# Kernel optimization log

Measured on AMD Instinct MI355X. Metric: run time of the kernel, lower is better.

## Reference

```python
import jax, jax.numpy as jnp
import numpy as np

B, C, H, W = 4, 64, 160, 160
K = 3
KK = K * K
PAD = (K - 1) // 2
EPS = 1e-5


def conv2d(x, w, b):
    y = jax.lax.conv_general_dilated(
        x, w, (1, 1), [(PAD, PAD), (PAD, PAD)],
        dimension_numbers=('NCHW', 'OIHW', 'NCHW'))
    return y + b[None, :, None, None]


def batchnorm(x, g, b, m, v):
    # eval-mode BN with running stats
    return (x - m[None, :, None, None]) * jax.lax.rsqrt(v + EPS)[None, :, None, None] * g[None, :, None, None] + b[None, :, None, None]


def bilinear_gather(x, py, px):
    # x: [B,C,H,W]; py,px: [B,KK,H,W] float sample coords -> [B,C,KK,H,W]
    Bx, Cx, Hx, Wx = x.shape
    y0 = jnp.floor(py)
    x0 = jnp.floor(px)
    ly = py - y0
    lx = px - x0
    x_flat = x.reshape(Bx, Cx, 1, Hx * Wx)
    acc = jnp.zeros((Bx, Cx, py.shape[1], Hx * Wx), dtype=x.dtype)
    corners = ((y0, x0, (1 - ly) * (1 - lx)),
               (y0, x0 + 1, (1 - ly) * lx),
               (y0 + 1, x0, ly * (1 - lx)),
               (y0 + 1, x0 + 1, ly * lx))
    for yi, xi, wgt in corners:
        valid = (yi >= 0) & (yi < Hx) & (xi >= 0) & (xi < Wx)
        yc = jnp.clip(yi, 0, Hx - 1).astype(jnp.int32)
        xc = jnp.clip(xi, 0, Wx - 1).astype(jnp.int32)
        idx = (yc * Wx + xc).reshape(Bx, -1, Hx * Wx)          # [B,KK,HW]
        g = jnp.take_along_axis(x_flat, idx[:, None], axis=3)  # [B,C,KK,HW]
        acc = acc + (wgt * valid).reshape(Bx, 1, -1, Hx * Wx) * g
    return acc.reshape(Bx, Cx, -1, Hx, Wx)


def modulated_deform_conv(x, offset, mask, weight):
    # x:[B,C,H,W] offset:[B,2*KK,H,W] (mmcv layout: pairs (dy,dx) interleaved) mask:[B,KK,H,W]
    Bx, Cx, Hx, Wx = x.shape
    Co = weight.shape[0]
    off = offset.reshape(Bx, KK, 2, Hx, Wx)
    k = jnp.arange(KK)
    ki = (k // K).astype(x.dtype)
    kj = (k % K).astype(x.dtype)
    ys = jnp.arange(Hx, dtype=x.dtype)
    xs = jnp.arange(Wx, dtype=x.dtype)
    py = ys[None, None, :, None] - PAD + ki[None, :, None, None] + off[:, :, 0]
    px = xs[None, None, None, :] - PAD + kj[None, :, None, None] + off[:, :, 1]
    samp = bilinear_gather(x, py, px)            # [B,C,KK,H,W]
    samp = samp * mask[:, None]                  # modulation
    return jnp.einsum('bckhw,ock->bohw', samp, weight.reshape(Co, Cx, KK))


def setup_inputs() -> dict:
    key = jax.random.key(0)
    ks = jax.random.split(key, 16)
    inp = {
        'x': jax.random.normal(ks[0], (B, C, H, W), jnp.float32),
        'w_om1': jax.random.normal(ks[1], (3 * KK, C, K, K), jnp.float32) * 0.01,
        'b_om1': jax.random.normal(ks[2], (3 * KK,), jnp.float32) * 0.01,
        'w_dcn1': jax.random.normal(ks[3], (C, C, K, K), jnp.float32) * 0.04,
        'bn1_g': jax.random.uniform(ks[4], (C,), jnp.float32, 0.5, 1.5),
        'bn1_b': jax.random.normal(ks[5], (C,), jnp.float32) * 0.1,
        'bn1_m': jax.random.normal(ks[6], (C,), jnp.float32) * 0.1,
        'bn1_v': jax.random.uniform(ks[7], (C,), jnp.float32, 0.5, 1.5),
        'w_om2': jax.random.normal(ks[8], (3 * KK, C, K, K), jnp.float32) * 0.01,
        'b_om2': jax.random.normal(ks[9], (3 * KK,), jnp.float32) * 0.01,
        'w_dcn2': jax.random.normal(ks[10], (C, C, K, K), jnp.float32) * 0.04,
        'bn2_g': jax.random.uniform(ks[11], (C,), jnp.float32, 0.5, 1.5),
        'bn2_b': jax.random.normal(ks[12], (C,), jnp.float32) * 0.1,
        'bn2_m': jax.random.normal(ks[13], (C,), jnp.float32) * 0.1,
        'bn2_v': jax.random.uniform(ks[14], (C,), jnp.float32, 0.5, 1.5),
    }
    return inp


def reference(x, w_om1, b_om1, w_dcn1, bn1_g, bn1_b, bn1_m, bn1_v,
              w_om2, b_om2, w_dcn2, bn2_g, bn2_b, bn2_m, bn2_v):
    identity = x
    om1 = conv2d(x, w_om1, b_om1)
    o1, o2, m1 = jnp.split(om1, 3, axis=1)
    offset1 = jnp.concatenate([o1, o2], axis=1)
    mask1 = jax.nn.sigmoid(m1)
    out = modulated_deform_conv(x, offset1, mask1, w_dcn1)
    out = batchnorm(out, bn1_g, bn1_b, bn1_m, bn1_v)
    out = jax.nn.gelu(out, approximate=False)
    om2 = conv2d(out, w_om2, b_om2)
    o1b, o2b, m2 = jnp.split(om2, 3, axis=1)
    offset2 = jnp.concatenate([o1b, o2b], axis=1)
    mask2 = jax.nn.sigmoid(m2)
    out = modulated_deform_conv(out, offset2, mask2, w_dcn2)
    out = batchnorm(out, bn2_g, bn2_b, bn2_m, bn2_v)
    out = out + identity
    return jax.nn.gelu(out, approximate=False)
```

## Files before the change

kernel.cpp:

```cpp
#include <hip/hip_runtime.h>
#include <math.h>

#define HH 160
#define WW 160
#define HWSZ 25600
#define TR 14
#define TC 22
#define NSLOT 308

typedef __attribute__((ext_vector_type(8))) short short8;
typedef __attribute__((ext_vector_type(4))) short short4v;
typedef __attribute__((ext_vector_type(8))) _Float16 half8;
typedef __attribute__((ext_vector_type(2))) _Float16 half2v;
typedef __attribute__((ext_vector_type(4))) float f32x4;
typedef __attribute__((ext_vector_type(16))) float f32x16;

__device__ __forceinline__ short f2h(float f) {
  union { _Float16 h; short s; } u; u.h = (_Float16)f; return u.s;
}
__device__ __forceinline__ float h2f(short s) {
  union { _Float16 h; short s; } u; u.s = s; return (float)u.h;
}
__device__ __forceinline__ half2v bcast_h(short s) {
  unsigned int x = (unsigned short)s; x |= x << 16;
  union { unsigned int u; half2v h; } v; v.u = x; return v.h;
}

__global__ __launch_bounds__(256) void pre_kernel(
    const float* __restrict__ x,
    const float* __restrict__ g1, const float* __restrict__ b1,
    const float* __restrict__ m1, const float* __restrict__ v1,
    const float* __restrict__ g2, const float* __restrict__ b2,
    const float* __restrict__ m2, const float* __restrict__ v2,
    const float* __restrict__ wd1, const float* __restrict__ wd2,
    const float* __restrict__ wo1, const float* __restrict__ wo2,
    float* __restrict__ sc, short* __restrict__ wd1h, short* __restrict__ wd2h,
    short* __restrict__ wo1h, short* __restrict__ wo2h,
    short* __restrict__ xcl) {
  __shared__ short tmp[64][72];
  int t = threadIdx.x;
  int bx = blockIdx.x;
  if (bx < 1600) {
    int b = bx / 400, p0 = (bx - b * 400) * 64;
    const float* xb = x + (size_t)b * 64 * HWSZ;
    for (int i = t; i < 4096; i += 256) {
      int c = i >> 6, p = i & 63;
      tmp[p][c] = f2h(xb[c * HWSZ + p0 + p]);
    }
    __syncthreads();
    short* ob = xcl + ((size_t)b * HWSZ + p0) * 64;
    for (int i = t; i < 512; i += 256) {
      int p = i >> 3, g = i & 7;
      *(short8*)&ob[p * 64 + g * 8] = *(const short8*)&tmp[p][g * 8];
    }
    return;
  }
  int i0 = (bx - 1600) * 256 + t;
  for (int i = i0; i < 36864; i += 16384) {
    int j = i & 7, oc = (i >> 3) & 31, hi = (i >> 8) & 1;
    int ot = (i >> 9) & 1, s = (i >> 10) & 3, tap = i >> 12;
    int src = (ot * 32 + oc) * 576 + (s * 16 + hi * 8 + j) * 9 + tap;
    wd1h[i] = f2h(wd1[src]);
    wd2h[i] = f2h(wd2[src]);
  }
  for (int i = i0; i < 18432; i += 16384) {
    int j = i & 7, q = (i >> 3) & 3, m = (i >> 5) & 15;
    int ot = (i >> 9) & 1, f = i >> 10;
    int kp = f * 32 + q * 8 + j;
    int k = kp >> 6, c = kp & 63;
    int oc = ot * 16 + m;
    wo1h[i] = (oc < 27) ? f2h(wo1[oc * 576 + c * 9 + k]) : (short)0;
    wo2h[i] = (oc < 27) ? f2h(wo2[oc * 576 + c * 9 + k]) : (short)0;
  }
  if (i0 < 64) {
    float s1 = g1[i0] * rsqrtf(v1[i0] + 1e-5f);
    sc[i0]       = s1;
    sc[64 + i0]  = b1[i0] - m1[i0] * s1;
    float s2 = g2[i0] * rsqrtf(v2[i0] + 1e-5f);
    sc[128 + i0] = s2;
    sc[192 + i0] = b2[i0] - m2[i0] * s2;
  }
}

__global__ __launch_bounds__(256, 2) void dcn_fused(
    const short* __restrict__ xcl,
    const short* __restrict__ who,
    const float* __restrict__ bias_om,
    const short* __restrict__ whd,
    const float* __restrict__ scale, const float* __restrict__ shift,
    const short* __restrict__ id_cl,
    short* __restrict__ out_cl,
    float* __restrict__ out_f32) {
  __shared__ short xt[NSLOT * 64];
  __shared__ __align__(16) short wA[12288];
  __shared__ __align__(16) short oms[4608];

  int t = threadIdx.x;
  int x0 = blockIdx.x * 16, y0 = blockIdx.y * 8, b = blockIdx.z;
  int w = t >> 6, lane = t & 63, q = lane >> 4, m = lane & 15;
  int hi = lane >> 5, p31 = lane & 31;
  int ybase = y0 - 3, xbase = x0 - 3;

  short8 pr[6];
#pragma unroll
  for (int c = 0; c < 6; c++)
    pr[c] = *(const short8*)&whd[c * 2048 + t * 8];

  const short* xb = xcl + (size_t)b * HWSZ * 64;
  for (int i = t; i < NSLOT * 8; i += 256) {
    int slot = i >> 3, g = i & 7;
    int ty = slot / TC, tx = slot - ty * TC;
    int gy = ybase + ty, gx = xbase + tx;
    short8 v = {};
    if (gy >= 0 && gy < HH && gx >= 0 && gx < WW)
      v = *(const short8*)&xb[(gy * WW + gx) * 64 + g * 8];
    *(short8*)&xt[slot * 64 + ((g ^ (slot & 7)) << 3)] = v;
  }
#pragma unroll
  for (int c = 0; c < 6; c++)
    *(short8*)&wA[c * 2048 + t * 8] = pr[c];
#pragma unroll
  for (int c = 0; c < 6; c++)
    pr[c] = *(const short8*)&whd[12288 + c * 2048 + t * 8];
  __syncthreads();

  {
    f32x4 oacc[2][2] = {};
#pragma unroll 6
    for (int f = 0; f < 18; f++) {
      int k = f >> 1;
      int ki = k / 3, kj = k - ki * 3;
      int g = (f & 1) * 4 + q;
      const short* ap = who + (f * 128 + m * 4 + q) * 8;
      short8 a0 = *(const short8*)ap;
      short8 a1 = *(const short8*)(ap + 512);
      union { short8 s8; half8 h; } A0, A1;
      A0.s8 = a0; A1.s8 = a1;
#pragma unroll
      for (int p = 0; p < 2; p++) {
        int slotb = (w * 2 + p + ki + 2) * TC + (m + kj + 2);
        union { short8 s8; half8 h; } B;
        B.s8 = *(const short8*)&xt[slotb * 64 + ((g ^ (slotb & 7)) << 3)];
        oacc[p][0] = __builtin_amdgcn_mfma_f32_16x16x32_f16(A0.h, B.h, oacc[p][0], 0, 0, 0);
        oacc[p][1] = __builtin_amdgcn_mfma_f32_16x16x32_f16(A1.h, B.h, oacc[p][1], 0, 0, 0);
      }
    }
#pragma unroll
    for (int p = 0; p < 2; p++) {
      int px = w * 32 + p * 16 + m;
#pragma unroll
      for (int mt = 0; mt < 2; mt++) {
        short4v pv;
#pragma unroll
        for (int r = 0; r < 4; r++) {
          int oc = mt * 16 + q * 4 + r;
          float bb = (oc < 27) ? bias_om[oc] : 0.f;
          pv[r] = f2h(oacc[p][mt][r] + bb);
        }
        *(short4v*)&oms[px * 36 + mt * 16 + q * 4] = pv;
      }
    }
  }
  __syncthreads();

  union { short s[36]; short4v v4[9]; } omr;
  {
    int px = w * 32 + p31;
#pragma unroll
    for (int i = 0; i < 9; i++)
      omr.v4[i] = *(const short4v*)&oms[px * 36 + i * 4];
  }

  int y = y0 + w * 2 + (p31 >> 4), x = x0 + m;

  short4v ivs[8];
  if (out_f32) {
    size_t pbase = ((size_t)b * HWSZ + y * WW + x) * 64;
#pragma unroll
    for (int ot = 0; ot < 2; ot++)
#pragma unroll
      for (int blk = 0; blk < 4; blk++)
        ivs[ot * 4 + blk] =
            *(const short4v*)&id_cl[pbase + ot * 32 + blk * 8 + hi * 4];
  }

  f32x16 acc0 = {}, acc1 = {};
#pragma unroll
  for (int grp = 0; grp < 3; ++grp) {
    if (grp > 0) {
      __syncthreads();
#pragma unroll
      for (int c = 0; c < 6; c++)
        *(short8*)&wA[c * 2048 + t * 8] = pr[c];
      if (grp < 2) {
#pragma unroll
        for (int c = 0; c < 6; c++)
          pr[c] = *(const short8*)&whd[(grp + 1) * 12288 + c * 2048 + t * 8];
      }
      __syncthreads();
    }
#pragma unroll
    for (int kt = 0; kt < 3; ++kt) {
      const int k = grp * 3 + kt;
      float dy = h2f(omr.s[2 * k]);
      float dx = h2f(omr.s[2 * k + 1]);
      float ml = h2f(omr.s[18 + k]);
      float msk = 1.f / (1.f + __expf(-ml));
      int ki = k / 3, kj = k - ki * 3;
      float py  = (float)(y - 1 + ki) + dy;
      float pxf = (float)(x - 1 + kj) + dx;
      float fy = floorf(py), fx = floorf(pxf);
      float ly = py - fy, lx = pxf - fx;
      int yi0 = (int)fy, xi0 = (int)fx;
      bool vy0 = (yi0 >= 0) & (yi0 < HH), vy1 = (yi0 + 1 >= 0) & (yi0 + 1 < HH);
      bool vx0 = (xi0 >= 0) & (xi0 < WW), vx1 = (xi0 + 1 >= 0) & (xi0 + 1 < WW);
      int ty0 = min(max(yi0 - ybase, 0), TR - 2);
      int tx0 = min(max(xi0 - xbase, 0), TC - 2);
      int p00 = ty0 * TC + tx0;
      half2v w00 = bcast_h(f2h((vy0 & vx0) ? (1.f - ly) * (1.f - lx) * msk : 0.f));
      half2v w01 = bcast_h(f2h((vy0 & vx1) ? (1.f - ly) * lx * msk : 0.f));
      half2v w10 = bcast_h(f2h((vy1 & vx0) ? ly * (1.f - lx) * msk : 0.f));
      half2v w11 = bcast_h(f2h((vy1 & vx1) ? ly * lx * msk : 0.f));
      int s00 = p00, s01 = p00 + 1, s10 = p00 + TC, s11 = p00 + TC + 1;
#pragma unroll
      for (int s = 0; s < 4; s++) {
        int g = s * 2 + hi;
        union { short8 s8; half2v h[4]; } c00, c01, c10, c11, bb;
        c00.s8 = *(const short8*)&xt[s00 * 64 + ((g ^ (s00 & 7)) << 3)];
        c01.s8 = *(const short8*)&xt[s01 * 64 + ((g ^ (s01 & 7)) << 3)];
        c10.s8 = *(const short8*)&xt[s10 * 64 + ((g ^ (s10 & 7)) << 3)];
        c11.s8 = *(const short8*)&xt[s11 * 64 + ((g ^ (s11 & 7)) << 3)];
#pragma unroll
        for (int d = 0; d < 4; d++)
          bb.h[d] = c00.h[d] * w00 + c01.h[d] * w01 + c10.h[d] * w10 +
                    c11.h[d] * w11;
        const short* ap = wA + kt * 4096 + s * 1024 + lane * 8;
        short8 a0 = *(const short8*)ap;
        short8 a1 = *(const short8*)(ap + 512);
        union { short8 s8; half8 h8; } B, A0, A1;
        B.s8 = bb.s8; A0.s8 = a0; A1.s8 = a1;
        acc0 = __builtin_amdgcn_mfma_f32_32x32x16_f16(A0.h8, B.h8, acc0, 0, 0, 0);
        acc1 = __builtin_amdgcn_mfma_f32_32x32x16_f16(A1.h8, B.h8, acc1, 0, 0, 0);
      }
    }
  }

  if (out_f32) {
#pragma unroll
    for (int ot = 0; ot < 2; ot++) {
#pragma unroll
      for (int r = 0; r < 16; r++) {
        int oc = ot * 32 + (r & 3) + 8 * (r >> 2) + 4 * hi;
        float a = ot ? acc1[r] : acc0[r];
        size_t idx = ((size_t)(b * 64 + oc)) * HWSZ + y * WW + x;
        float v = a * scale[oc] + shift[oc] + h2f(ivs[ot * 4 + (r >> 2)][r & 3]);
        v = 0.5f * v * (1.f + erff(v * 0.70710678118654752f));
        out_f32[idx] = v;
      }
    }
  } else {
    size_t base = ((size_t)b * HWSZ + y * WW + x) * 64;
#pragma unroll
    for (int ot = 0; ot < 2; ot++) {
#pragma unroll
      for (int blk = 0; blk < 4; blk++) {
        short4v pv;
#pragma unroll
        for (int rr = 0; rr < 4; rr++) {
          int r = blk * 4 + rr;
          int oc = ot * 32 + blk * 8 + hi * 4 + rr;
          float a = ot ? acc1[r] : acc0[r];
          float v = a * scale[oc] + shift[oc];
          v = 0.5f * v * (1.f + erff(v * 0.70710678118654752f));
          pv[rr] = f2h(v);
        }
        *(short4v*)&out_cl[base + ot * 32 + blk * 8 + hi * 4] = pv;
      }
    }
  }
}

extern "C" void kernel_launch(void* const* d_in, const int* in_sizes, int n_in,
                              void* d_out, int out_size, void* d_ws, size_t ws_size,
                              hipStream_t stream) {
  const float* x     = (const float*)d_in[0];
  const float* w_om1 = (const float*)d_in[1];
  const float* b_om1 = (const float*)d_in[2];
  const float* w_d1  = (const float*)d_in[3];
  const float* bn1g  = (const float*)d_in[4];
  const float* bn1b  = (const float*)d_in[5];
  const float* bn1m  = (const float*)d_in[6];
  const float* bn1v  = (const float*)d_in[7];
  const float* w_om2 = (const float*)d_in[8];
  const float* b_om2 = (const float*)d_in[9];
  const float* w_d2  = (const float*)d_in[10];
  const float* bn2g  = (const float*)d_in[11];
  const float* bn2b  = (const float*)d_in[12];
  const float* bn2m  = (const float*)d_in[13];
  const float* bn2v  = (const float*)d_in[14];

  float* ws    = (float*)d_ws;
  float* sc    = ws;
  short* w1h   = (short*)(ws + 256);
  short* w2h   = w1h + 36864;
  short* wo1h  = w2h + 36864;
  short* wo2h  = wo1h + 18432;
  short* x_cl  = (short*)(ws + 55552);
  short* o1_cl = x_cl + 6553600;
  float* outp  = (float*)d_out;

  pre_kernel<<<dim3(1664), dim3(256), 0, stream>>>(
      x, bn1g, bn1b, bn1m, bn1v, bn2g, bn2b, bn2m, bn2v,
      w_d1, w_d2, w_om1, w_om2, sc, w1h, w2h, wo1h, wo2h, x_cl);

  dim3 grid(WW / 16, HH / 8, 4);
  dcn_fused<<<grid, dim3(256), 0, stream>>>(
      x_cl, wo1h, b_om1, w1h, sc, sc + 64, nullptr, o1_cl, nullptr);
  dcn_fused<<<grid, dim3(256), 0, stream>>>(
      o1_cl, wo2h, b_om2, w2h, sc + 128, sc + 192, x_cl, nullptr, outp);
}
```

Measured before the change: 209.0 us.

## Shrink weight staging to one tap and union LDS to fit three blocks per CU

```diff
diff --git a/kernel.cpp b/kernel.cpp
--- a/kernel.cpp
+++ b/kernel.cpp
@@ -82,7 +82,7 @@
   }
 }
 
-__global__ __launch_bounds__(256, 2) void dcn_fused(
+__global__ __launch_bounds__(256, 3) void dcn_fused(
     const short* __restrict__ xcl,
     const short* __restrict__ who,
     const float* __restrict__ bias_om,
@@ -92,8 +92,7 @@
     short* __restrict__ out_cl,
     float* __restrict__ out_f32) {
   __shared__ short xt[NSLOT * 64];
-  __shared__ __align__(16) short wA[12288];
-  __shared__ __align__(16) short oms[4608];
+  __shared__ __align__(16) short uni[5120];
 
   int t = threadIdx.x;
   int x0 = blockIdx.x * 16, y0 = blockIdx.y * 8, b = blockIdx.z;
@@ -101,10 +100,8 @@
   int hi = lane >> 5, p31 = lane & 31;
   int ybase = y0 - 3, xbase = x0 - 3;
 
-  short8 pr[6];
-#pragma unroll
-  for (int c = 0; c < 6; c++)
-    pr[c] = *(const short8*)&whd[c * 2048 + t * 8];
+  short8 pr0 = *(const short8*)&whd[t * 8];
+  short8 pr1 = *(const short8*)&whd[2048 + t * 8];
 
   const short* xb = xcl + (size_t)b * HWSZ * 64;
   for (int i = t; i < NSLOT * 8; i += 256) {
@@ -116,12 +113,6 @@
       v = *(const short8*)&xb[(gy * WW + gx) * 64 + g * 8];
     *(short8*)&xt[slot * 64 + ((g ^ (slot & 7)) << 3)] = v;
   }
-#pragma unroll
-  for (int c = 0; c < 6; c++)
-    *(short8*)&wA[c * 2048 + t * 8] = pr[c];
-#pragma unroll
-  for (int c = 0; c < 6; c++)
-    pr[c] = *(const short8*)&whd[12288 + c * 2048 + t * 8];
   __syncthreads();
 
   {
@@ -157,19 +148,26 @@
           float bb = (oc < 27) ? bias_om[oc] : 0.f;
           pv[r] = f2h(oacc[p][mt][r] + bb);
         }
-        *(short4v*)&oms[px * 36 + mt * 16 + q * 4] = pv;
+        *(short4v*)&uni[px * 40 + mt * 16 + q * 4] = pv;
       }
     }
   }
   __syncthreads();
 
-  union { short s[36]; short4v v4[9]; } omr;
+  union { short s[40]; short8 v8[5]; } omr;
   {
     int px = w * 32 + p31;
 #pragma unroll
-    for (int i = 0; i < 9; i++)
-      omr.v4[i] = *(const short4v*)&oms[px * 36 + i * 4];
-  }
+    for (int i = 0; i < 5; i++)
+      omr.v8[i] = *(const short8*)&uni[px * 40 + i * 8];
+  }
+  __syncthreads();
+
+  *(short8*)&uni[t * 8]        = pr0;
+  *(short8*)&uni[2048 + t * 8] = pr1;
+  pr0 = *(const short8*)&whd[4096 + t * 8];
+  pr1 = *(const short8*)&whd[4096 + 2048 + t * 8];
+  __syncthreads();
 
   int y = y0 + w * 2 + (p31 >> 4), x = x0 + m;
 
@@ -186,62 +184,56 @@
 
   f32x16 acc0 = {}, acc1 = {};
 #pragma unroll
-  for (int grp = 0; grp < 3; ++grp) {
-    if (grp > 0) {
+  for (int k = 0; k < 9; ++k) {
+    float dy = h2f(omr.s[2 * k]);
+    float dx = h2f(omr.s[2 * k + 1]);
+    float ml = h2f(omr.s[18 + k]);
+    float msk = 1.f / (1.f + __expf(-ml));
+    int ki = k / 3, kj = k - ki * 3;
+    float py  = (float)(y - 1 + ki) + dy;
+    float pxf = (float)(x - 1 + kj) + dx;
+    float fy = floorf(py), fx = floorf(pxf);
+    float ly = py - fy, lx = pxf - fx;
+    int yi0 = (int)fy, xi0 = (int)fx;
+    bool vy0 = (yi0 >= 0) & (yi0 < HH), vy1 = (yi0 + 1 >= 0) & (yi0 + 1 < HH);
+    bool vx0 = (xi0 >= 0) & (xi0 < WW), vx1 = (xi0 + 1 >= 0) & (xi0 + 1 < WW);
+    int ty0 = min(max(yi0 - ybase, 0), TR - 2);
+    int tx0 = min(max(xi0 - xbase, 0), TC - 2);
+    int p00 = ty0 * TC + tx0;
+    half2v w00 = bcast_h(f2h((vy0 & vx0) ? (1.f - ly) * (1.f - lx) * msk : 0.f));
+    half2v w01 = bcast_h(f2h((vy0 & vx1) ? (1.f - ly) * lx * msk : 0.f));
+    half2v w10 = bcast_h(f2h((vy1 & vx0) ? ly * (1.f - lx) * msk : 0.f));
+    half2v w11 = bcast_h(f2h((vy1 & vx1) ? ly * lx * msk : 0.f));
+    int s00 = p00, s01 = p00 + 1, s10 = p00 + TC, s11 = p00 + TC + 1;
+#pragma unroll
+    for (int s = 0; s < 4; s++) {
+      int g = s * 2 + hi;
+      union { short8 s8; half2v h[4]; } c00, c01, c10, c11, bb;
+      c00.s8 = *(const short8*)&xt[s00 * 64 + ((g ^ (s00 & 7)) << 3)];
+      c01.s8 = *(const short8*)&xt[s01 * 64 + ((g ^ (s01 & 7)) << 3)];
+      c10.s8 = *(const short8*)&xt[s10 * 64 + ((g ^ (s10 & 7)) << 3)];
+      c11.s8 = *(const short8*)&xt[s11 * 64 + ((g ^ (s11 & 7)) << 3)];
+#pragma unroll
+      for (int d = 0; d < 4; d++)
+        bb.h[d] = c00.h[d] * w00 + c01.h[d] * w01 + c10.h[d] * w10 +
+                  c11.h[d] * w11;
+      const short* ap = uni + s * 1024 + lane * 8;
+      short8 a0 = *(const short8*)ap;
+      short8 a1 = *(const short8*)(ap + 512);
+      union { short8 s8; half8 h8; } B, A0, A1;
+      B.s8 = bb.s8; A0.s8 = a0; A1.s8 = a1;
+      acc0 = __builtin_amdgcn_mfma_f32_32x32x16_f16(A0.h8, B.h8, acc0, 0, 0, 0);
+      acc1 = __builtin_amdgcn_mfma_f32_32x32x16_f16(A1.h8, B.h8, acc1, 0, 0, 0);
+    }
+    if (k < 8) {
       __syncthreads();
-#pragma unroll
-      for (int c = 0; c < 6; c++)
-        *(short8*)&wA[c * 2048 + t * 8] = pr[c];
-      if (grp < 2) {
-#pragma unroll
-        for (int c = 0; c < 6; c++)
-          pr[c] = *(const short8*)&whd[(grp + 1) * 12288 + c * 2048 + t * 8];
+      *(short8*)&uni[t * 8]        = pr0;
+      *(short8*)&uni[2048 + t * 8] = pr1;
+      if (k < 7) {
+        pr0 = *(const short8*)&whd[(k + 2) * 4096 + t * 8];
+        pr1 = *(const short8*)&whd[(k + 2) * 4096 + 2048 + t * 8];
       }
       __syncthreads();
-    }
-#pragma unroll
-    for (int kt = 0; kt < 3; ++kt) {
-      const int k = grp * 3 + kt;
-      float dy = h2f(omr.s[2 * k]);
-      float dx = h2f(omr.s[2 * k + 1]);
-      float ml = h2f(omr.s[18 + k]);
-      float msk = 1.f / (1.f + __expf(-ml));
-      int ki = k / 3, kj = k - ki * 3;
-      float py  = (float)(y - 1 + ki) + dy;
-      float pxf = (float)(x - 1 + kj) + dx;
-      float fy = floorf(py), fx = floorf(pxf);
-      float ly = py - fy, lx = pxf - fx;
-      int yi0 = (int)fy, xi0 = (int)fx;
-      bool vy0 = (yi0 >= 0) & (yi0 < HH), vy1 = (yi0 + 1 >= 0) & (yi0 + 1 < HH);
-      bool vx0 = (xi0 >= 0) & (xi0 < WW), vx1 = (xi0 + 1 >= 0) & (xi0 + 1 < WW);
-      int ty0 = min(max(yi0 - ybase, 0), TR - 2);
-      int tx0 = min(max(xi0 - xbase, 0), TC - 2);
-      int p00 = ty0 * TC + tx0;
-      half2v w00 = bcast_h(f2h((vy0 & vx0) ? (1.f - ly) * (1.f - lx) * msk : 0.f));
-      half2v w01 = bcast_h(f2h((vy0 & vx1) ? (1.f - ly) * lx * msk : 0.f));
-      half2v w10 = bcast_h(f2h((vy1 & vx0) ? ly * (1.f - lx) * msk : 0.f));
-      half2v w11 = bcast_h(f2h((vy1 & vx1) ? ly * lx * msk : 0.f));
-      int s00 = p00, s01 = p00 + 1, s10 = p00 + TC, s11 = p00 + TC + 1;
-#pragma unroll
-      for (int s = 0; s < 4; s++) {
-        int g = s * 2 + hi;
-        union { short8 s8; half2v h[4]; } c00, c01, c10, c11, bb;
-        c00.s8 = *(const short8*)&xt[s00 * 64 + ((g ^ (s00 & 7)) << 3)];
-        c01.s8 = *(const short8*)&xt[s01 * 64 + ((g ^ (s01 & 7)) << 3)];
-        c10.s8 = *(const short8*)&xt[s10 * 64 + ((g ^ (s10 & 7)) << 3)];
-        c11.s8 = *(const short8*)&xt[s11 * 64 + ((g ^ (s11 & 7)) << 3)];
-#pragma unroll
-        for (int d = 0; d < 4; d++)
-          bb.h[d] = c00.h[d] * w00 + c01.h[d] * w01 + c10.h[d] * w10 +
-                    c11.h[d] * w11;
-        const short* ap = wA + kt * 4096 + s * 1024 + lane * 8;
-        short8 a0 = *(const short8*)ap;
-        short8 a1 = *(const short8*)(ap + 512);
-        union { short8 s8; half8 h8; } B, A0, A1;
-        B.s8 = bb.s8; A0.s8 = a0; A1.s8 = a1;
-        acc0 = __builtin_amdgcn_mfma_f32_32x32x16_f16(A0.h8, B.h8, acc0, 0, 0, 0);
-        acc1 = __builtin_amdgcn_mfma_f32_32x32x16_f16(A1.h8, B.h8, acc1, 0, 0, 0);
-      }
     }
   }
 
```

New measurement: 200.0 us. 4.3% less time.
